# Kernel optimization log

Measured on AMD Instinct MI355X. Metric: run time of the kernel, lower is better.

Reference implementation:

```python
import jax, jax.numpy as jnp
import numpy as np

B, N, D = 32, 4096, 512


def setup_inputs() -> dict:
    key0 = jax.random.key(0)
    kq, kk, kv, ks = jax.random.split(key0, 4)
    query = jax.random.normal(kq, (B, D), dtype=jnp.float32)
    key = jax.random.normal(kk, (B, N, D), dtype=jnp.float32)
    # Plant a few query-aligned candidates so cosine sim exceeds the 0.9 threshold
    # for some entries (otherwise random vectors give ~0 cosine and attn is all zero).
    scale = jax.random.uniform(ks, (B, 8, 1), minval=2.0, maxval=5.0)
    key = key.at[:, :8, :].set(scale * query[:, None, :] + 0.01 * key[:, :8, :])
    value = jax.random.normal(kv, (B, N, D), dtype=jnp.float32)
    mask = jnp.zeros((B, N), dtype=bool)
    return {"query": query, "key": key, "value": value, "mask": mask}


def reference(query, key, value, mask):
    # dot_product: bmm(key [B,N,D], query [B,D,1]) -> [B,N]
    dot = jnp.einsum("bnd,bd->bn", key, query)
    norm_q = jnp.linalg.norm(query, axis=1)          # [B]
    norm_k = jnp.linalg.norm(key, axis=2)            # [B,N]
    denom = jnp.clip(norm_q[:, None] * norm_k, 1e-8, None)
    attn = dot / denom                               # cosine similarity [B,N]
    attn = jnp.where(mask, 0.0, attn)                # masked_fill_(mask, 0)
    attn = jnp.where(attn < 0.9, 0.0, attn)          # hard threshold
    attn = attn / (jnp.sum(attn, axis=1, keepdims=True) + 1e-8)
    # weighted_context: bmm(attn [B,1,N], value [B,N,Dv]) -> [B,Dv]
    return jnp.einsum("bn,bnd->bd", attn, value)
```

## Files before the change

### kernel.cpp

```cpp
#include <hip/hip_runtime.h>
#include <math.h>

#define BB 32
#define NN 4096
#define DD 512
#define ROWS_PER_WAVE 16

typedef float v4f __attribute__((ext_vector_type(4)));

__device__ __forceinline__ float half_reduce_add(float v) {
    v += __shfl_xor(v, 16, 64);
    v += __shfl_xor(v, 8, 64);
    v += __shfl_xor(v, 4, 64);
    v += __shfl_xor(v, 2, 64);
    v += __shfl_xor(v, 1, 64);
    return v;
}

__device__ __forceinline__ float dot4(v4f a, v4f b) {
    return a.x * b.x + a.y * b.y + a.z * b.z + a.w * b.w;
}

__global__ __launch_bounds__(256) void sim_pass1_kernel(
    const float* __restrict__ q, const float* __restrict__ key,
    const unsigned char* __restrict__ mask,
    int* __restrict__ count, int2* __restrict__ list)
{
    const int lane = threadIdx.x & 63;
    const int half = lane >> 5;
    const int l32  = lane & 31;
    const int wave = threadIdx.x >> 6;
    const int wg   = blockIdx.x * (blockDim.x >> 6) + wave;
    const int r0   = wg * ROWS_PER_WAVE;
    const int b    = r0 >> 12;

    const v4f* qr = reinterpret_cast<const v4f*>(q + (size_t)b * DD);
    v4f qv0 = qr[l32 + 0];
    v4f qv1 = qr[l32 + 32];
    v4f qv2 = qr[l32 + 64];
    v4f qv3 = qr[l32 + 96];
    float qq = dot4(qv0, qv0) + dot4(qv1, qv1) + dot4(qv2, qv2) + dot4(qv3, qv3);
    qq = half_reduce_add(qq);
    const float qn = sqrtf(qq);

#pragma unroll 2
    for (int i = 0; i < ROWS_PER_WAVE / 2; ++i) {
        const int row = r0 + 2 * i + half;
        const v4f* kr = reinterpret_cast<const v4f*>(key + (size_t)row * DD);
        v4f k0 = __builtin_nontemporal_load(&kr[l32 + 0]);
        v4f k1 = __builtin_nontemporal_load(&kr[l32 + 32]);
        v4f k2 = __builtin_nontemporal_load(&kr[l32 + 64]);
        v4f k3 = __builtin_nontemporal_load(&kr[l32 + 96]);

        float dot = dot4(k0, qv0) + dot4(k1, qv1) + dot4(k2, qv2) + dot4(k3, qv3);
        float kk  = dot4(k0, k0) + dot4(k1, k1) + dot4(k2, k2) + dot4(k3, k3);

        dot = half_reduce_add(dot);
        kk  = half_reduce_add(kk);

        if (l32 == 0) {
            float denom = fmaxf(qn * sqrtf(kk), 1e-8f);
            float attn  = dot / denom;
            if (attn >= 0.9f && mask[row] == 0) {
                int idx = atomicAdd(&count[b], 1);
                list[(size_t)b * NN + idx] = make_int2(row & (NN - 1), __float_as_int(attn));
            }
        }
    }
}

__global__ __launch_bounds__(512) void sim_pass2_kernel(
    const float* __restrict__ value, const int* __restrict__ count,
    const int2* __restrict__ list, float* __restrict__ out)
{
    const int b = blockIdx.x;
    const int d = threadIdx.x;
    const int c = count[b];
    float asum = 0.0f;
    float acc  = 0.0f;
    for (int i = 0; i < c; ++i) {
        int2 e = list[(size_t)b * NN + i];
        float a = __int_as_float(e.y);
        asum += a;
        acc  += a * value[((size_t)b * NN + e.x) * DD + d];
    }
    out[(size_t)b * DD + d] = acc / (asum + 1e-8f);
}

extern "C" void kernel_launch(void* const* d_in, const int* in_sizes, int n_in,
                              void* d_out, int out_size, void* d_ws, size_t ws_size,
                              hipStream_t stream) {
    const float* query = (const float*)d_in[0];
    const float* key   = (const float*)d_in[1];
    const float* value = (const float*)d_in[2];
    const unsigned char* mask = (const unsigned char*)d_in[3];
    float* out = (float*)d_out;

    char* ws = (char*)d_ws;
    int*  count = (int*)(ws);
    int2* list  = (int2*)(ws + 256);

    (void)hipMemsetAsync(count, 0, BB * sizeof(int), stream);
    sim_pass1_kernel<<<2048, 256, 0, stream>>>(query, key, mask, count, list);
    sim_pass2_kernel<<<BB, DD, 0, stream>>>(value, count, list, out);
}
```

Before: 54.68 us.

## Replace global atomics with per-wave compacted lists and DPP reductions

Pass 1 now writes each wave's passing rows into its own fixed slot range, with a ballot-based offset and a per-wave count, instead of using a global atomic counter per batch. This also removes the memset launch. The cross-lane reductions switch from shuffles to DPP row operations, with lane 31 of each half holding the sum. Pass 2 walks the 256 per-wave counts of its batch in int4 chunks, which adds 256 count reads per block but gives a deterministic order.

```diff
diff --git a/kernel.cpp b/kernel.cpp
--- a/kernel.cpp
+++ b/kernel.cpp
@@ -5,15 +5,21 @@
 #define NN 4096
 #define DD 512
 #define ROWS_PER_WAVE 16
+#define WAVES_TOTAL (BB * NN / ROWS_PER_WAVE)
+#define WAVES_PER_BATCH (NN / ROWS_PER_WAVE)
 
 typedef float v4f __attribute__((ext_vector_type(4)));
 
-__device__ __forceinline__ float half_reduce_add(float v) {
-    v += __shfl_xor(v, 16, 64);
-    v += __shfl_xor(v, 8, 64);
-    v += __shfl_xor(v, 4, 64);
-    v += __shfl_xor(v, 2, 64);
-    v += __shfl_xor(v, 1, 64);
+__device__ __forceinline__ float dpp_reduce_half32(float v) {
+#define DPP_ADD(ctrl) \
+    v += __int_as_float(__builtin_amdgcn_update_dpp( \
+        0, __float_as_int(v), ctrl, 0xF, 0xF, true))
+    DPP_ADD(0x111);
+    DPP_ADD(0x112);
+    DPP_ADD(0x114);
+    DPP_ADD(0x118);
+    DPP_ADD(0x142);
+#undef DPP_ADD
     return v;
 }
 
@@ -24,7 +30,7 @@
 __global__ __launch_bounds__(256) void sim_pass1_kernel(
     const float* __restrict__ q, const float* __restrict__ key,
     const unsigned char* __restrict__ mask,
-    int* __restrict__ count, int2* __restrict__ list)
+    int* __restrict__ wcount, int2* __restrict__ list)
 {
     const int lane = threadIdx.x & 63;
     const int half = lane >> 5;
@@ -40,8 +46,11 @@
     v4f qv2 = qr[l32 + 64];
     v4f qv3 = qr[l32 + 96];
     float qq = dot4(qv0, qv0) + dot4(qv1, qv1) + dot4(qv2, qv2) + dot4(qv3, qv3);
-    qq = half_reduce_add(qq);
+    qq = dpp_reduce_half32(qq);
     const float qn = sqrtf(qq);
+
+    const bool leader = (l32 == 31);
+    int base = 0;
 
 #pragma unroll 2
     for (int i = 0; i < ROWS_PER_WAVE / 2; ++i) {
@@ -55,34 +64,53 @@
         float dot = dot4(k0, qv0) + dot4(k1, qv1) + dot4(k2, qv2) + dot4(k3, qv3);
         float kk  = dot4(k0, k0) + dot4(k1, k1) + dot4(k2, k2) + dot4(k3, k3);
 
-        dot = half_reduce_add(dot);
-        kk  = half_reduce_add(kk);
+        dot = dpp_reduce_half32(dot);
+        kk  = dpp_reduce_half32(kk);
 
-        if (l32 == 0) {
+        bool pass = false;
+        float attn = 0.0f;
+        if (leader) {
             float denom = fmaxf(qn * sqrtf(kk), 1e-8f);
-            float attn  = dot / denom;
-            if (attn >= 0.9f && mask[row] == 0) {
-                int idx = atomicAdd(&count[b], 1);
-                list[(size_t)b * NN + idx] = make_int2(row & (NN - 1), __float_as_int(attn));
-            }
+            attn = dot / denom;
+            pass = (attn >= 0.9f) && (mask[row] == 0);
         }
+        unsigned long long bal = __ballot(pass);
+        int lo = (int)((bal >> 31) & 1ull);
+        int hi = (int)((bal >> 63) & 1ull);
+        if (pass) {
+            int slot = base + ((lane == 63) ? lo : 0);
+            list[(size_t)wg * ROWS_PER_WAVE + slot] =
+                make_int2(row & (NN - 1), __float_as_int(attn));
+        }
+        base += lo + hi;
     }
+
+    if (lane == 0) wcount[wg] = base;
 }
 
 __global__ __launch_bounds__(512) void sim_pass2_kernel(
-    const float* __restrict__ value, const int* __restrict__ count,
+    const float* __restrict__ value, const int* __restrict__ wcount,
     const int2* __restrict__ list, float* __restrict__ out)
 {
     const int b = blockIdx.x;
     const int d = threadIdx.x;
-    const int c = count[b];
+    const int wbase = b * WAVES_PER_BATCH;
     float asum = 0.0f;
     float acc  = 0.0f;
-    for (int i = 0; i < c; ++i) {
-        int2 e = list[(size_t)b * NN + i];
-        float a = __int_as_float(e.y);
-        asum += a;
-        acc  += a * value[((size_t)b * NN + e.x) * DD + d];
+    for (int w0 = 0; w0 < WAVES_PER_BATCH; w0 += 4) {
+        int4 c4 = *reinterpret_cast<const int4*>(&wcount[wbase + w0]);
+#pragma unroll
+        for (int k = 0; k < 4; ++k) {
+            int c = (k == 0) ? c4.x : (k == 1) ? c4.y : (k == 2) ? c4.z : c4.w;
+            if (c == 0) continue;
+            const int2* lw = &list[(size_t)(wbase + w0 + k) * ROWS_PER_WAVE];
+            for (int j = 0; j < c; ++j) {
+                int2 e = lw[j];
+                float a = __int_as_float(e.y);
+                asum += a;
+                acc  += a * value[((size_t)b * NN + e.x) * DD + d];
+            }
+        }
     }
     out[(size_t)b * DD + d] = acc / (asum + 1e-8f);
 }
@@ -97,10 +125,10 @@
     float* out = (float*)d_out;
 
     char* ws = (char*)d_ws;
-    int*  count = (int*)(ws);
-    int2* list  = (int2*)(ws + 256);
+    int*  wcount = (int*)(ws);
+    int2* list   = (int2*)(ws + WAVES_TOTAL * 4);
 
-    (void)hipMemsetAsync(count, 0, BB * sizeof(int), stream);
-    sim_pass1_kernel<<<2048, 256, 0, stream>>>(query, key, mask, count, list);
-    sim_pass2_kernel<<<BB, DD, 0, stream>>>(value, count, list, out);
+    sim_pass1_kernel<<<WAVES_TOTAL / 4, 256, 0, stream>>>(query, key, mask,
+                                                          wcount, list);
+    sim_pass2_kernel<<<BB, DD, 0, stream>>>(value, wcount, list, out);
 }
```

After: 59.72 us. +9.2%, slower.

## Fuse weighted value accumulation into scan kernel with per-block partials

Applied to the files above, without the earlier changes.

Each scan block now collects its above-threshold entries in shared memory and immediately accumulates the weighted value rows into a per-block partial, which a small combine kernel then reduces per batch. This removes the global atomic list, the memset, and the serial per-batch gather loop of the old second pass. Rows are interleaved across blocks so that candidates spread over blocks. It adds a partial-sum write and read plus a block barrier, and the 64-entry shared buffer assumes at most 64 hits per block, which overflows if a block finds more.

```diff
diff --git a/kernel.cpp b/kernel.cpp
--- a/kernel.cpp
+++ b/kernel.cpp
@@ -5,6 +5,8 @@
 #define NN 4096
 #define DD 512
 #define ROWS_PER_WAVE 16
+#define WAVES_TOTAL (BB * NN / ROWS_PER_WAVE)
+#define BLOCKS_PER_BATCH 64
 
 typedef float v4f __attribute__((ext_vector_type(4)));
 
@@ -21,18 +23,24 @@
     return a.x * b.x + a.y * b.y + a.z * b.z + a.w * b.w;
 }
 
-__global__ __launch_bounds__(256) void sim_pass1_kernel(
+__global__ __launch_bounds__(256) void sim_scan_kernel(
     const float* __restrict__ q, const float* __restrict__ key,
-    const unsigned char* __restrict__ mask,
-    int* __restrict__ count, int2* __restrict__ list)
+    const unsigned char* __restrict__ mask, const float* __restrict__ value,
+    float* __restrict__ partial, float* __restrict__ asum_p)
 {
+    __shared__ int  s_cnt;
+    __shared__ int2 s_ent[BLOCKS_PER_BATCH];
+
     const int lane = threadIdx.x & 63;
     const int half = lane >> 5;
     const int l32  = lane & 31;
     const int wave = threadIdx.x >> 6;
-    const int wg   = blockIdx.x * (blockDim.x >> 6) + wave;
-    const int r0   = wg * ROWS_PER_WAVE;
-    const int b    = r0 >> 12;
+    const int wg   = blockIdx.x * 4 + wave;
+    const int b    = wg >> 8;
+    const int w    = wg & 255;
+
+    if (threadIdx.x == 0) s_cnt = 0;
+    __syncthreads();
 
     const v4f* qr = reinterpret_cast<const v4f*>(q + (size_t)b * DD);
     v4f qv0 = qr[l32 + 0];
@@ -43,10 +51,13 @@
     qq = half_reduce_add(qq);
     const float qn = sqrtf(qq);
 
+    const bool leader = (l32 == 0);
+
 #pragma unroll 2
     for (int i = 0; i < ROWS_PER_WAVE / 2; ++i) {
-        const int row = r0 + 2 * i + half;
-        const v4f* kr = reinterpret_cast<const v4f*>(key + (size_t)row * DD);
+        const int n = 512 * i + 2 * w + half;
+        const size_t row = (size_t)b * NN + n;
+        const v4f* kr = reinterpret_cast<const v4f*>(key + row * DD);
         v4f k0 = __builtin_nontemporal_load(&kr[l32 + 0]);
         v4f k1 = __builtin_nontemporal_load(&kr[l32 + 32]);
         v4f k2 = __builtin_nontemporal_load(&kr[l32 + 64]);
@@ -58,33 +69,51 @@
         dot = half_reduce_add(dot);
         kk  = half_reduce_add(kk);
 
-        if (l32 == 0) {
+        if (leader) {
             float denom = fmaxf(qn * sqrtf(kk), 1e-8f);
             float attn  = dot / denom;
             if (attn >= 0.9f && mask[row] == 0) {
-                int idx = atomicAdd(&count[b], 1);
-                list[(size_t)b * NN + idx] = make_int2(row & (NN - 1), __float_as_int(attn));
+                int slot = atomicAdd(&s_cnt, 1);
+                s_ent[slot] = make_int2(n, __float_as_int(attn));
             }
         }
     }
+
+    __syncthreads();
+
+    const int t = threadIdx.x;
+    const int c = s_cnt;
+    float asum = 0.0f, acc0 = 0.0f, acc1 = 0.0f;
+    const float* vb = value + (size_t)b * NN * DD;
+    for (int j = 0; j < c; ++j) {
+        int2 e = s_ent[j];
+        float a = __int_as_float(e.y);
+        asum += a;
+        const float* vr = vb + (size_t)e.x * DD;
+        acc0 += a * vr[t];
+        acc1 += a * vr[t + 256];
+    }
+    float* pr = partial + (size_t)blockIdx.x * DD;
+    pr[t]       = acc0;
+    pr[t + 256] = acc1;
+    if (t == 0) asum_p[blockIdx.x] = asum;
 }
 
-__global__ __launch_bounds__(512) void sim_pass2_kernel(
-    const float* __restrict__ value, const int* __restrict__ count,
-    const int2* __restrict__ list, float* __restrict__ out)
+__global__ __launch_bounds__(512) void sim_combine_kernel(
+    const float* __restrict__ partial, const float* __restrict__ asum_p,
+    float* __restrict__ out)
 {
     const int b = blockIdx.x;
     const int d = threadIdx.x;
-    const int c = count[b];
-    float asum = 0.0f;
-    float acc  = 0.0f;
-    for (int i = 0; i < c; ++i) {
-        int2 e = list[(size_t)b * NN + i];
-        float a = __int_as_float(e.y);
-        asum += a;
-        acc  += a * value[((size_t)b * NN + e.x) * DD + d];
-    }
-    out[(size_t)b * DD + d] = acc / (asum + 1e-8f);
+    float s = 0.0f;
+#pragma unroll 8
+    for (int j = 0; j < BLOCKS_PER_BATCH; ++j)
+        s += partial[(size_t)(b * BLOCKS_PER_BATCH + j) * DD + d];
+    float a = 0.0f;
+#pragma unroll 8
+    for (int j = 0; j < BLOCKS_PER_BATCH; ++j)
+        a += asum_p[b * BLOCKS_PER_BATCH + j];
+    out[(size_t)b * DD + d] = s / (a + 1e-8f);
 }
 
 extern "C" void kernel_launch(void* const* d_in, const int* in_sizes, int n_in,
@@ -97,10 +126,10 @@
     float* out = (float*)d_out;
 
     char* ws = (char*)d_ws;
-    int*  count = (int*)(ws);
-    int2* list  = (int2*)(ws + 256);
+    float* partial = (float*)(ws);
+    float* asum_p  = (float*)(ws + (size_t)WAVES_TOTAL / 4 * DD * 4);
 
-    (void)hipMemsetAsync(count, 0, BB * sizeof(int), stream);
-    sim_pass1_kernel<<<2048, 256, 0, stream>>>(query, key, mask, count, list);
-    sim_pass2_kernel<<<BB, DD, 0, stream>>>(value, count, list, out);
+    sim_scan_kernel<<<WAVES_TOTAL / 4, 256, 0, stream>>>(query, key, mask, value,
+                                                         partial, asum_p);
+    sim_combine_kernel<<<BB, DD, 0, stream>>>(partial, asum_p, out);
 }
```

Result: faster. 52.29 us (-4.4%).
